# Kernel optimization log

Measured on AMD Instinct MI355X. Metric: run time of the kernel, lower is better.

Reference implementation:

```python
import math
import jax, jax.numpy as jnp
import numpy as np

N = 2048          # batch size
D = 256           # embedding_dim
MEM = 16384       # memory_size
ANOMALY_WEIGHT = 1.0
TEMP = 0.1
MOMENTUM = 0.01
NCLS = 2          # binary phishing labels -> max(labels.max()+1, 2) == 2


def setup_inputs() -> dict:
    key = jax.random.key(0)
    ks = jax.random.split(key, 10)
    s = 1.0 / math.sqrt(D)  # nn.Linear default init range
    return {
        'z': jax.random.normal(ks[0], (N, D), jnp.float32),
        'labels': jax.random.randint(ks[1], (N,), 0, NCLS),
        'memory': jax.random.normal(ks[2], (MEM, D), jnp.float32),
        'memory_weights': jax.random.uniform(ks[3], (MEM,), jnp.float32),
        'running_mean': jnp.zeros((D,), jnp.float32),
        'running_cov': jnp.eye(D, dtype=jnp.float32),
        'Wq': jax.random.uniform(ks[4], (D, D), jnp.float32, -s, s),
        'bq': jax.random.uniform(ks[5], (D,), jnp.float32, -s, s),
        'Wk': jax.random.uniform(ks[6], (D, D), jnp.float32, -s, s),
        'bk': jax.random.uniform(ks[7], (D,), jnp.float32, -s, s),
        'Wv': jax.random.uniform(ks[8], (D, D), jnp.float32, -s, s),
        'bv': jax.random.uniform(ks[9], (D,), jnp.float32, -s, s),
    }


def reference(z, labels, memory, memory_weights, running_mean, running_cov,
              Wq, bq, Wk, bk, Wv, bv):
    # ---- update(z.detach(), labels): entire update path is detached in torch ----
    z_sg = jax.lax.stop_gradient(z)

    # _update_stats: EMA of batch mean / covariance (done before importance)
    mu = z_sg.mean(axis=0)                                  # [D]
    zc = z_sg - mu
    cov = zc.T @ zc / max(N - 1, 1)                         # [D, D]
    rm = (1.0 - MOMENTUM) * running_mean + MOMENTUM * mu
    rc = (1.0 - MOMENTUM) * running_cov + MOMENTUM * cov

    # _mahalanobis with updated running stats
    c = z_sg - rm
    cov_inv = jnp.linalg.inv(rc + 1e-6 * jnp.eye(D, dtype=rc.dtype))
    dist = jnp.sqrt(jnp.clip(jnp.einsum('nd,de,ne->n', c, cov_inv, c), 1e-8))
    a_norm = (dist - dist.min()) / (dist.max() - dist.min() + 1e-8)

    # _mi_proxy: KL(batch label dist || uniform), broadcast to all items
    counts = jnp.zeros((NCLS,), z.dtype).at[labels].add(1.0)
    p = counts / jnp.clip(counts.sum(), 1.0)
    # p / uniform == p * NCLS; clip inside log for safety (both classes present)
    kl = jnp.clip((p * jnp.log(jnp.clip(p * NCLS, 1e-8))).sum(), 0.0)
    importance = (1.0 + ANOMALY_WEIGHT * a_norm) * kl       # [N]

    # serial top-1 priority-queue eviction, in descending-importance order
    order = jnp.argsort(-importance)
    z_ord = z_sg[order]
    imp_ord = importance[order]

    def evict_step(state, inp):
        mem, w = state
        zi, imp = inp
        j = jnp.argmin(w)                   # weakest memory slot
        rep = imp > w[j]
        mem = mem.at[j].set(jnp.where(rep, zi, mem[j]))
        w = w.at[j].set(jnp.where(rep, imp, w[j]))
        return (mem, w), None

    (mem, _), _ = jax.lax.scan(evict_step, (memory, memory_weights), (z_ord, imp_ord))

    # ---- query(z): cross-attention over the (full) updated memory ----
    Q = z @ Wq.T + bq                       # [N, D]
    K = mem @ Wk.T + bk                     # [MEM, D]
    V = mem @ Wv.T + bv                     # [MEM, D]
    sc = (Q @ K.T) / math.sqrt(D)           # [N, MEM]
    attn = jax.nn.softmax(sc / TEMP, axis=-1)
    return z + 0.5 * (attn @ V)
```

## Files before the change

kernel.cpp:

```cpp
#include <hip/hip_runtime.h>
#include <math.h>

#define NB   2048
#define DE   256
#define MEMN 16384
#define CAND_CAP 256
#define FSPL 32
#define FKPS 512
#define FIT  16

typedef __attribute__((ext_vector_type(8)))  short  short8;
typedef __attribute__((ext_vector_type(16))) float  float16;
typedef __attribute__((ext_vector_type(4)))  unsigned uint4v;
typedef __attribute__((ext_vector_type(2)))  unsigned uint2v;

static const size_t OFF_QB   = 0;
static const size_t OFF_KB   = 262144;
static const size_t OFF_VTB  = 2359296;
static const size_t OFF_LP   = 4456448;
static const size_t OFF_OPB  = 4521984;
static const size_t SO_APART = 0;
static const size_t SO_A     = 1048576;
static const size_t SO_MUP   = 1114112;
static const size_t SO_DIST  = 1130496;

__device__ inline unsigned short f2bf(float f) {
  unsigned u = __float_as_uint(f);
  unsigned r = (u + 0x7fffu + ((u >> 16) & 1u)) >> 16;
  return (unsigned short)r;
}
__device__ inline float bf2f(unsigned short s) {
  return __uint_as_float((unsigned)s << 16);
}

__device__ inline unsigned cvtpk_bf16(float lo, float hi) {
  unsigned r;
  asm("v_cvt_pk_bf16_f32 %0, %1, %2" : "=v"(r) : "v"(lo), "v"(hi));
  return r;
}
__device__ inline short8 pack8_bf16(float4 f0, float4 f1) {
  uint4v u = {cvtpk_bf16(f0.x, f0.y), cvtpk_bf16(f0.z, f0.w),
              cvtpk_bf16(f1.x, f1.y), cvtpk_bf16(f1.z, f1.w)};
  return __builtin_bit_cast(short8, u);
}

__device__ inline void halfswap(unsigned& lo, unsigned& hi, int h) {
#if __has_builtin(__builtin_amdgcn_permlane32_swap)
  (void)h;
  uint2v r = __builtin_amdgcn_permlane32_swap(lo, hi, false, false);
  lo = r.x; hi = r.y;
#else
  unsigned a = (unsigned)__shfl_xor((int)lo, 32, 64);
  unsigned b = (unsigned)__shfl_xor((int)hi, 32, 64);
  unsigned nlo = (h == 0) ? lo : b;
  unsigned nhi = (h == 0) ? a  : hi;
  lo = nlo; hi = nhi;
#endif
}

__device__ inline void bitonic_sort_u64(unsigned long long* key, int n, int tid, int nth) {
  for (int k = 2; k <= n; k <<= 1) {
    for (int j = k >> 1; j > 0; j >>= 1) {
      __syncthreads();
      for (int i = tid; i < n; i += nth) {
        int ixj = i ^ j;
        if (ixj > i) {
          unsigned long long a = key[i], b = key[ixj];
          bool up = ((i & k) == 0);
          if ((a > b) == up) { key[i] = b; key[ixj] = a; }
        }
      }
    }
  }
  __syncthreads();
}

__global__ __launch_bounds__(256) void covmu_kernel(const float* __restrict__ z,
                                                    float* __restrict__ Apart,
                                                    float* __restrict__ mup,
                                                    const float* __restrict__ Wq,
                                                    const float* __restrict__ bq,
                                                    unsigned short* __restrict__ Qbf) {
  int f = blockIdx.x;
  int tid = threadIdx.x;
  if (f >= 320) {
    __shared__ unsigned short Bsh[64 * 264];
    int g = f - 320;
    int gx = g & 15, gy = g >> 4;
    int w = tid >> 6, lane = tid & 63;
    int m = lane & 31, h = lane >> 5;
    int arow = gx * 128 + w * 32 + m;
    int n0 = gy * 64;
    short8 af[16];
#pragma unroll
    for (int kc = 0; kc < 16; ++kc) {
      const float* src = &z[(size_t)arow * DE + kc * 16 + h * 8];
      af[kc] = pack8_bf16(*(const float4*)&src[0], *(const float4*)&src[4]);
    }
    {
      int r = tid >> 2, q = tid & 3;
      const float* src = &Wq[(size_t)(n0 + r) * DE + q * 64];
      unsigned short* dst = &Bsh[r * 264 + q * 64];
#pragma unroll
      for (int j = 0; j < 8; ++j)
        *(short8*)&dst[j * 8] = pack8_bf16(*(const float4*)&src[j * 8],
                                           *(const float4*)&src[j * 8 + 4]);
    }
    __syncthreads();
    float16 a0 = {}, a1 = {};
#pragma unroll
    for (int kc = 0; kc < 16; ++kc) {
      short8 b0 = *(const short8*)&Bsh[(0 * 32 + m) * 264 + kc * 16 + h * 8];
      short8 b1 = *(const short8*)&Bsh[(1 * 32 + m) * 264 + kc * 16 + h * 8];
      a0 = __builtin_amdgcn_mfma_f32_32x32x16_bf16(af[kc], b0, a0, 0, 0, 0);
      a1 = __builtin_amdgcn_mfma_f32_32x32x16_bf16(af[kc], b1, a1, 0, 0, 0);
    }
#pragma unroll
    for (int r = 0; r < 16; ++r) {
      int rr = (r & 3) + 8 * (r >> 2) + 4 * h;
      int orow = gx * 128 + w * 32 + rr;
      int oc0 = n0 + m, oc1 = n0 + 32 + m;
      Qbf[(size_t)orow * DE + oc0] = f2bf(a0[r] + bq[oc0]);
      Qbf[(size_t)orow * DE + oc1] = f2bf(a1[r] + bq[oc1]);
    }
    return;
  }
  if (f >= 256) {
    int b = f - 256;
    int r0 = b * 32;
    float s = 0.f;
    for (int r = 0; r < 32; ++r) s += z[(size_t)(r0 + r) * DE + tid];
    mup[b * DE + tid] = s;
    return;
  }
  __shared__ float As[16][68];
  __shared__ float Bs[16][68];
  int tx = tid & 15, ty = tid >> 4;
  int i0 = (f & 3) * 64, j0 = ((f >> 2) & 3) * 64;
  int slice = f >> 4;
  int nbase = slice * 128;
  float acc[4][4] = {};
  for (int nt = 0; nt < 8; ++nt) {
    int n0 = nbase + nt * 16;
    for (int e = tid; e < 1024; e += 256) {
      int c = e & 63, nn = e >> 6;
      As[nn][c] = z[(size_t)(n0 + nn) * DE + i0 + c];
      Bs[nn][c] = z[(size_t)(n0 + nn) * DE + j0 + c];
    }
    __syncthreads();
#pragma unroll
    for (int nn = 0; nn < 16; ++nn) {
      float4 a4 = *(const float4*)&As[nn][ty * 4];
      float4 b4 = *(const float4*)&Bs[nn][tx * 4];
      acc[0][0] += a4.x*b4.x; acc[0][1] += a4.x*b4.y; acc[0][2] += a4.x*b4.z; acc[0][3] += a4.x*b4.w;
      acc[1][0] += a4.y*b4.x; acc[1][1] += a4.y*b4.y; acc[1][2] += a4.y*b4.z; acc[1][3] += a4.y*b4.w;
      acc[2][0] += a4.z*b4.x; acc[2][1] += a4.z*b4.y; acc[2][2] += a4.z*b4.z; acc[2][3] += a4.z*b4.w;
      acc[3][0] += a4.w*b4.x; acc[3][1] += a4.w*b4.y; acc[3][2] += a4.w*b4.z; acc[3][3] += a4.w*b4.w;
    }
    __syncthreads();
  }
  float* dstA = &Apart[(size_t)slice * 65536];
  for (int r = 0; r < 4; ++r) {
    int i = i0 + ty * 4 + r;
    for (int c = 0; c < 4; ++c) {
      int j = j0 + tx * 4 + c;
      dstA[(size_t)i * DE + j] = acc[r][c];
    }
  }
}

__global__ __launch_bounds__(256) void covred_kernel(const float* __restrict__ Apart,
                                                     float* __restrict__ A) {
  int e0 = (blockIdx.x * 256 + threadIdx.x) * 4;
  float4 s = {0.f, 0.f, 0.f, 0.f};
#pragma unroll
  for (int sl = 0; sl < 16; ++sl) {
    float4 v = *(const float4*)&Apart[(size_t)sl * 65536 + e0];
    s.x += v.x; s.y += v.y; s.z += v.z; s.w += v.w;
  }
  *(float4*)&A[e0] = s;
}

__global__ __launch_bounds__(256) void dist_kernel(const float* __restrict__ z,
                                                   const float* __restrict__ rmean,
                                                   const float* __restrict__ mup,
                                                   const float* __restrict__ ZtZ,
                                                   const float* __restrict__ rcov,
                                                   float* __restrict__ dist) {
  __shared__ float cc[8][256];
  __shared__ float mus[256];
  __shared__ float4 red[256];
  int n0 = blockIdx.x * 8, i = threadIdx.x;
  float s = 0.f;
  for (int b = 0; b < 64; ++b) s += mup[b * DE + i];
  mus[i] = s;
  float rmi = 0.99f * rmean[i] + 0.01f * s * (1.0f / (float)NB);
#pragma unroll
  for (int r = 0; r < 8; ++r) cc[r][i] = z[(size_t)(n0 + r) * DE + i] - rmi;
  __syncthreads();
  const float c1 = 0.01f / (float)(NB - 1);
  const float invN = 1.0f / (float)NB;
  float musi = mus[i];
  float u[8] = {};
#pragma unroll 4
  for (int j = 0; j < DE; ++j) {
    float base = 0.99f * rcov[(size_t)j * DE + i] +
                 c1 * (ZtZ[(size_t)j * DE + i] - mus[j] * musi * invN);
    float e = -base;
    if (j == i) e += 1.0f - 1e-6f;
#pragma unroll
    for (int r = 0; r < 8; ++r) u[r] += e * cc[r][j];
  }
  {
    float4 v;
    v.x = cc[0][i] * (cc[0][i] + u[0]) + u[0] * u[0];
    v.y = cc[1][i] * (cc[1][i] + u[1]) + u[1] * u[1];
    v.z = cc[2][i] * (cc[2][i] + u[2]) + u[2] * u[2];
    v.w = cc[3][i] * (cc[3][i] + u[3]) + u[3] * u[3];
    red[i] = v;
    __syncthreads();
    for (int sH = 128; sH > 0; sH >>= 1) {
      if (i < sH) {
        float4 a = red[i], b = red[i + sH];
        a.x += b.x; a.y += b.y; a.z += b.z; a.w += b.w;
        red[i] = a;
      }
      __syncthreads();
    }
    if (i < 4) {
      float4 tt = red[0];
      float d = (i == 0) ? tt.x : (i == 1) ? tt.y : (i == 2) ? tt.z : tt.w;
      dist[n0 + i] = sqrtf(fmaxf(d, 1e-8f));
    }
    __syncthreads();
  }
  {
    float4 v;
    v.x = cc[4][i] * (cc[4][i] + u[4]) + u[4] * u[4];
    v.y = cc[5][i] * (cc[5][i] + u[5]) + u[5] * u[5];
    v.z = cc[6][i] * (cc[6][i] + u[6]) + u[6] * u[6];
    v.w = cc[7][i] * (cc[7][i] + u[7]) + u[7] * u[7];
    red[i] = v;
    __syncthreads();
    for (int sH = 128; sH > 0; sH >>= 1) {
      if (i < sH) {
        float4 a = red[i], b = red[i + sH];
        a.x += b.x; a.y += b.y; a.z += b.z; a.w += b.w;
        red[i] = a;
      }
      __syncthreads();
    }
    if (i < 4) {
      float4 tt = red[0];
      float d = (i == 0) ? tt.x : (i == 1) ? tt.y : (i == 2) ? tt.z : tt.w;
      dist[n0 + 4 + i] = sqrtf(fmaxf(d, 1e-8f));
    }
  }
}

__global__ __launch_bounds__(1024) void update_kernel(const float* __restrict__ dist,
                                                      const int* __restrict__ labels,
                                                      const float* __restrict__ weights,
                                                      const float* __restrict__ z,
                                                      float* __restrict__ memory) {
  __shared__ unsigned long long ikeys[NB];
  __shared__ unsigned long long ck[CAND_CAP];
  __shared__ unsigned long long gmin[16];
  __shared__ int slots[CAND_CAP], srcs[CAND_CAP];
  __shared__ float smin[16], smax[16];
  __shared__ int scnt[16];
  __shared__ float s_kl, s_dmin, s_inv;
  __shared__ int s_ccnt, s_m, s_stop, s_bg;
  int t = threadIdx.x;
  int wid = t >> 6, lane = t & 63;

  float mn = 1e30f, mx = -1e30f; int c1 = 0;
  for (int n = t; n < NB; n += 1024) {
    float d = dist[n];
    mn = fminf(mn, d); mx = fmaxf(mx, d);
    c1 += labels[n];
  }
#pragma unroll
  for (int o = 32; o > 0; o >>= 1) {
    mn = fminf(mn, __shfl_xor(mn, o, 64));
    mx = fmaxf(mx, __shfl_xor(mx, o, 64));
    c1 += __shfl_xor(c1, o, 64);
  }
  if (lane == 0) { smin[wid] = mn; smax[wid] = mx; scnt[wid] = c1; }
  if (t == 0) { s_ccnt = 0; s_m = 0; s_stop = 0; }
  __syncthreads();
  if (t == 0) {
    float a = 1e30f, b = -1e30f; int cc = 0;
    for (int i = 0; i < 16; ++i) { a = fminf(a, smin[i]); b = fmaxf(b, smax[i]); cc += scnt[i]; }
    float p1 = (float)cc / (float)NB;
    float p0 = (float)(NB - cc) / (float)NB;
    float kl = p0 * logf(fmaxf(2.f * p0, 1e-8f)) + p1 * logf(fmaxf(2.f * p1, 1e-8f));
    s_kl = fmaxf(kl, 0.f);
    s_dmin = a;
    s_inv = 1.0f / (b - a + 1e-8f);
  }
  __syncthreads();
  float kl = s_kl;

  for (int n = t; n < NB; n += 1024) {
    float imp = (1.0f + (dist[n] - s_dmin) * s_inv) * kl;
    ikeys[n] = ((unsigned long long)(unsigned)(~__float_as_uint(imp)) << 32) | (unsigned)n;
  }
  float thresh = 2.f * kl;
  for (int j = t; j < MEMN; j += 1024) {
    float wv = weights[j];
    if (wv < thresh) {
      int p = atomicAdd(&s_ccnt, 1);
      if (p < CAND_CAP) ck[p] = ((unsigned long long)__float_as_uint(wv) << 32) | (unsigned)j;
    }
  }
  __syncthreads();
  int C = s_ccnt; if (C > CAND_CAP) C = CAND_CAP;
  for (int i = t; i < CAND_CAP; i += 1024)
    if (i >= C) ck[i] = 0xFFFFFFFFFFFFFFFFULL;
  __syncthreads();
  if (C <= 64) {
    if (wid == 0) {
      unsigned long long key = (lane < C) ? ck[lane] : 0xFFFFFFFFFFFFFFFFULL;
      int rank = 0;
      for (int j = 0; j < 64; ++j) {
        unsigned long long o = (unsigned long long)__shfl((long long)key, j, 64);
        rank += (o < key) || (o == key && j < lane);
      }
      if (lane < C) ck[rank] = key;
    }
    __syncthreads();
  } else {
    bitonic_sort_u64(ck, CAND_CAP, t, 1024);
  }

  {
    unsigned long long a = ikeys[wid * 128 + lane];
    unsigned long long b = ikeys[wid * 128 + 64 + lane];
    unsigned long long mm = a < b ? a : b;
#pragma unroll
    for (int o = 32; o > 0; o >>= 1) {
      unsigned long long ot = (unsigned long long)__shfl_xor((long long)mm, o, 64);
      if (ot < mm) mm = ot;
    }
    if (lane == 0) gmin[wid] = mm;
  }
  __syncthreads();

  float prevv = 0.f;
  for (int i = 0; i < C; ++i) {
    if (t == 0) {
      unsigned long long best = 0xFFFFFFFFFFFFFFFFULL;
      for (int g = 0; g < 16; ++g) if (gmin[g] < best) best = gmin[g];
      float im = __uint_as_float(~(unsigned)(best >> 32));
      float wv = __uint_as_float((unsigned)(ck[i] >> 32));
      bool ok = (im > wv) && (i == 0 || prevv >= wv);
      if (ok) {
        int idx = (int)(best & 0xffffffffULL);
        slots[s_m] = (int)(ck[i] & 0xffffffffULL);
        srcs[s_m]  = idx;
        s_m++;
        prevv = im;
        ikeys[idx] = 0xFFFFFFFFFFFFFFFFULL;
        s_bg = idx >> 7;
      } else {
        s_stop = 1; s_bg = -1;
      }
    }
    __syncthreads();
    if (s_stop) break;
    if (wid == s_bg) {
      unsigned long long a = ikeys[wid * 128 + lane];
      unsigned long long b = ikeys[wid * 128 + 64 + lane];
      unsigned long long mm = a < b ? a : b;
#pragma unroll
      for (int o = 32; o > 0; o >>= 1) {
        unsigned long long ot = (unsigned long long)__shfl_xor((long long)mm, o, 64);
        if (ot < mm) mm = ot;
      }
      if (lane == 0) gmin[wid] = mm;
    }
    __syncthreads();
  }
  int m = s_m;
  for (int e = t; e < m * DE; e += 1024) {
    int i = e >> 8, d = e & 255;
    memory[(size_t)slots[i] * DE + d] = z[(size_t)srcs[i] * DE + d];
  }
}

__global__ __launch_bounds__(256, 1) void qkv_kernel(
    const float* __restrict__ memory,
    const float* __restrict__ Wk, const float* __restrict__ bk,
    const float* __restrict__ Wv, const float* __restrict__ bv,
    unsigned short* __restrict__ Kbf, unsigned short* __restrict__ Vtb) {
  __shared__ unsigned short Bsh[64 * 264];
  int flat = blockIdx.x;
  int tid = threadIdx.x;
  int w = tid >> 6, lane = tid & 63;
  int m = lane & 31, h = lane >> 5;

  if (flat < 128) {
    int gx = flat;
    int arow = gx * 128 + w * 32 + m;
    short8 af[16];
#pragma unroll
    for (int kc = 0; kc < 16; ++kc) {
      const float* src = &memory[(size_t)arow * DE + kc * 16 + h * 8];
      af[kc] = pack8_bf16(*(const float4*)&src[0], *(const float4*)&src[4]);
    }
    for (int g4 = 0; g4 < 4; ++g4) {
      int n0 = g4 * 64;
      __syncthreads();
      {
        int r = tid >> 2, q = tid & 3;
        const float* src = &Wk[(size_t)(n0 + r) * DE + q * 64];
        unsigned short* dst = &Bsh[r * 264 + q * 64];
#pragma unroll
        for (int j = 0; j < 8; ++j)
          *(short8*)&dst[j * 8] = pack8_bf16(*(const float4*)&src[j * 8],
                                             *(const float4*)&src[j * 8 + 4]);
      }
      __syncthreads();
      float16 a0 = {}, a1 = {};
#pragma unroll
      for (int kc = 0; kc < 16; ++kc) {
        short8 b0 = *(const short8*)&Bsh[(0 * 32 + m) * 264 + kc * 16 + h * 8];
        short8 b1 = *(const short8*)&Bsh[(1 * 32 + m) * 264 + kc * 16 + h * 8];
        a0 = __builtin_amdgcn_mfma_f32_32x32x16_bf16(af[kc], b0, a0, 0, 0, 0);
        a1 = __builtin_amdgcn_mfma_f32_32x32x16_bf16(af[kc], b1, a1, 0, 0, 0);
      }
#pragma unroll
      for (int r = 0; r < 16; ++r) {
        int rr = (r & 3) + 8 * (r >> 2) + 4 * h;
        int orow = gx * 128 + w * 32 + rr;
        int oc0 = n0 + m, oc1 = n0 + 32 + m;
        Kbf[(size_t)orow * DE + oc0] = f2bf(a0[r] + bk[oc0]);
        Kbf[(size_t)orow * DE + oc1] = f2bf(a1[r] + bk[oc1]);
      }
    }
  } else {
    int gy = flat - 128;
    int n0 = gy * 64;
    {
      int r = tid >> 2, q = tid & 3;
      const float* src = &memory[(size_t)(n0 + r) * DE + q * 64];
      unsigned short* dst = &Bsh[r * 264 + q * 64];
#pragma unroll
      for (int j = 0; j < 8; ++j)
        *(short8*)&dst[j * 8] = pack8_bf16(*(const float4*)&src[j * 8],
                                           *(const float4*)&src[j * 8 + 4]);
    }
    __syncthreads();
    for (int gxv = 0; gxv < 2; ++gxv) {
      short8 af[16];
#pragma unroll
      for (int kc = 0; kc < 16; ++kc) {
        const float* src = &Wv[(size_t)(gxv * 128 + w * 32 + m) * DE + kc * 16 + h * 8];
        af[kc] = pack8_bf16(*(const float4*)&src[0], *(const float4*)&src[4]);
      }
      float16 a0 = {}, a1 = {};
#pragma unroll
      for (int kc = 0; kc < 16; ++kc) {
        short8 b0 = *(const short8*)&Bsh[(0 * 32 + m) * 264 + kc * 16 + h * 8];
        short8 b1 = *(const short8*)&Bsh[(1 * 32 + m) * 264 + kc * 16 + h * 8];
        a0 = __builtin_amdgcn_mfma_f32_32x32x16_bf16(af[kc], b0, a0, 0, 0, 0);
        a1 = __builtin_amdgcn_mfma_f32_32x32x16_bf16(af[kc], b1, a1, 0, 0, 0);
      }
#pragma unroll
      for (int r = 0; r < 16; ++r) {
        int rr = (r & 3) + 8 * (r >> 2) + 4 * h;
        int orow = gxv * 128 + w * 32 + rr;
        int oc0 = n0 + m, oc1 = n0 + 32 + m;
        Vtb[(size_t)(oc0 >> 5) * 8192 + (size_t)orow * 32 + (oc0 & 31)] = f2bf(a0[r] + bv[orow]);
        Vtb[(size_t)(oc1 >> 5) * 8192 + (size_t)orow * 32 + (oc1 & 31)] = f2bf(a1[r] + bv[orow]);
      }
    }
  }
}

__global__ __launch_bounds__(512, 2) void flash_kernel(
    const unsigned short* __restrict__ Qb, const unsigned short* __restrict__ Kb,
    const unsigned short* __restrict__ Vtb, unsigned short* __restrict__ Opb,
    float* __restrict__ Lp) {
  __shared__ unsigned short Ks[32 * 264];
  __shared__ unsigned short Vs[256 * 40];

  int tid = threadIdx.x;
  int w = tid >> 6, lane = tid & 63;
  int m = lane & 31, h = lane >> 5;
  int sp = blockIdx.x, qg = blockIdx.y;
  int myrow = qg * 256 + w * 32 + m;

  short8 qf[16];
#pragma unroll
  for (int kc = 0; kc < 16; ++kc)
    qf[kc] = *(const short8*)&Qb[(size_t)myrow * DE + kc * 16 + h * 8];

  float16 O[8] = {};
  float lacc = 0.f;

  short8 kreg[2], vreg[2];
#define LOAD_TILES(kb_)                                                              \
  {                                                                                  \
    int kb = (kb_);                                                                  \
    _Pragma("unroll")                                                                \
    for (int i = 0; i < 2; ++i) {                                                    \
      int c = i * 512 + tid, kr = c >> 5, kcol = c & 31;                             \
      kreg[i] = *(const short8*)&Kb[(size_t)(kb + kr) * DE + kcol * 8];              \
    }                                                                                \
    const unsigned short* vg = &Vtb[(size_t)((kb) >> 5) * 8192];                     \
    _Pragma("unroll")                                                                \
    for (int i = 0; i < 2; ++i) {                                                    \
      int c = i * 512 + tid;                                                         \
      vreg[i] = *(const short8*)&vg[c * 8];                                          \
    }                                                                                \
  }
#define STORE_TILES()                                                                \
  {                                                                                  \
    _Pragma("unroll")                                                                \
    for (int i = 0; i < 2; ++i) {                                                    \
      int c = i * 512 + tid, kr = c >> 5, kcol = c & 31;                             \
      *(short8*)&Ks[kr * 264 + kcol * 8] = kreg[i];                                  \
    }                                                                                \
    _Pragma("unroll")                                                                \
    for (int i = 0; i < 2; ++i) {                                                    \
      int c = i * 512 + tid, dr = c >> 2, dc = c & 3;                                \
      *(short8*)&Vs[dr * 40 + dc * 8] = vreg[i];                                     \
    }                                                                                \
  }

  LOAD_TILES(sp * FKPS);

  for (int it = 0; it < FIT; ++it) {
    __syncthreads();
    STORE_TILES();
    if (it + 1 < FIT) LOAD_TILES(sp * FKPS + (it + 1) * 32);
    __syncthreads();

    float16 s = {};
    __builtin_amdgcn_s_setprio(1);
#pragma unroll
    for (int kc = 0; kc < 16; ++kc) {
      short8 b0 = *(const short8*)&Ks[m * 264 + kc * 16 + h * 8];
      s = __builtin_amdgcn_mfma_f32_32x32x16_bf16(b0, qf[kc], s, 0, 0, 0);
    }
    __builtin_amdgcn_s_setprio(0);

    float p[16];
#pragma unroll
    for (int r = 0; r < 16; ++r)
      p[r] = exp2f(fmaf(s[r], 0.90168440f, -16.0f));

    lacc += ((p[0] + p[1]) + (p[2] + p[3])) + ((p[4] + p[5]) + (p[6] + p[7])) +
            ((p[8] + p[9]) + (p[10] + p[11])) + ((p[12] + p[13]) + (p[14] + p[15]));

    unsigned c0 = cvtpk_bf16(p[0],  p[1]);
    unsigned c1 = cvtpk_bf16(p[2],  p[3]);
    unsigned c2 = cvtpk_bf16(p[4],  p[5]);
    unsigned c3 = cvtpk_bf16(p[6],  p[7]);
    unsigned c4 = cvtpk_bf16(p[8],  p[9]);
    unsigned c5 = cvtpk_bf16(p[10], p[11]);
    unsigned c6 = cvtpk_bf16(p[12], p[13]);
    unsigned c7 = cvtpk_bf16(p[14], p[15]);
    halfswap(c0, c2, h);
    halfswap(c1, c3, h);
    halfswap(c4, c6, h);
    halfswap(c5, c7, h);
    uint4v w0v = {c0, c1, c2, c3};
    uint4v w1v = {c4, c5, c6, c7};
    short8 pa0 = __builtin_bit_cast(short8, w0v);
    short8 pa1 = __builtin_bit_cast(short8, w1v);

    __builtin_amdgcn_s_setprio(1);
#pragma unroll
    for (int ct = 0; ct < 8; ++ct) {
      short8 vb0 = *(const short8*)&Vs[(ct * 32 + m) * 40 + h * 8];
      short8 vb1 = *(const short8*)&Vs[(ct * 32 + m) * 40 + 16 + h * 8];
      O[ct] = __builtin_amdgcn_mfma_f32_32x32x16_bf16(pa0, vb0, O[ct], 0, 0, 0);
      O[ct] = __builtin_amdgcn_mfma_f32_32x32x16_bf16(pa1, vb1, O[ct], 0, 0, 0);
    }
    __builtin_amdgcn_s_setprio(0);
  }
#undef LOAD_TILES
#undef STORE_TILES

  size_t ob = ((size_t)sp * NB + qg * 256 + w * 32) * DE;
#pragma unroll
  for (int ct = 0; ct < 8; ++ct)
#pragma unroll
    for (int r = 0; r < 16; ++r) {
      int rr = (r & 3) + 8 * (r >> 2) + 4 * h;
      Opb[ob + (size_t)rr * DE + ct * 32 + m] = f2bf(O[ct][r]);
    }
  float ltot = lacc + __shfl_xor(lacc, 32, 64);
  if (h == 0)
    Lp[sp * NB + qg * 256 + w * 32 + m] = ltot;
}

__global__ __launch_bounds__(256) void combine_kernel(const float* __restrict__ z,
                                                      const unsigned short* __restrict__ Opb,
                                                      const float* __restrict__ Lp,
                                                      float* __restrict__ out) {
  int t = threadIdx.x;
  int n = blockIdx.x * 8 + (t >> 5);
  int c0 = (t & 31) * 8;
  float num[8] = {};
  float den = 0.f;
#pragma unroll
  for (int s = 0; s < FSPL; ++s) {
    den += Lp[s * NB + n];
    short8 v = *(const short8*)&Opb[((size_t)s * NB + n) * DE + c0];
#pragma unroll
    for (int j = 0; j < 8; ++j) num[j] += bf2f((unsigned short)v[j]);
  }
  size_t base = (size_t)n * DE + c0;
  float4 o0, o1;
  o0.x = z[base + 0] + 0.5f * num[0] / den;
  o0.y = z[base + 1] + 0.5f * num[1] / den;
  o0.z = z[base + 2] + 0.5f * num[2] / den;
  o0.w = z[base + 3] + 0.5f * num[3] / den;
  o1.x = z[base + 4] + 0.5f * num[4] / den;
  o1.y = z[base + 5] + 0.5f * num[5] / den;
  o1.z = z[base + 6] + 0.5f * num[6] / den;
  o1.w = z[base + 7] + 0.5f * num[7] / den;
  *(float4*)&out[base] = o0;
  *(float4*)&out[base + 4] = o1;
}

extern "C" void kernel_launch(void* const* d_in, const int* in_sizes, int n_in,
                              void* d_out, int out_size, void* d_ws, size_t ws_size,
                              hipStream_t stream) {
  (void)in_sizes; (void)n_in; (void)out_size; (void)ws_size;
  const float* z       = (const float*)d_in[0];
  const int*   labels  = (const int*)d_in[1];
  float*       memory  = (float*)d_in[2];
  const float* weights = (const float*)d_in[3];
  const float* rmean   = (const float*)d_in[4];
  const float* rcov    = (const float*)d_in[5];
  const float* Wq      = (const float*)d_in[6];
  const float* bq      = (const float*)d_in[7];
  const float* Wk      = (const float*)d_in[8];
  const float* bk      = (const float*)d_in[9];
  const float* Wv      = (const float*)d_in[10];
  const float* bv      = (const float*)d_in[11];
  float* out = (float*)d_out;
  float* ws  = (float*)d_ws;

  unsigned short* Qbf = (unsigned short*)(ws + OFF_QB);
  unsigned short* Kbf = (unsigned short*)(ws + OFF_KB);
  unsigned short* Vtb = (unsigned short*)(ws + OFF_VTB);
  float* Lp           = ws + OFF_LP;
  unsigned short* Opb = (unsigned short*)(ws + OFF_OPB);
  float* SB    = ws + OFF_OPB;
  float* Apart = SB + SO_APART;
  float* A     = SB + SO_A;
  float* mup   = SB + SO_MUP;
  float* dist  = SB + SO_DIST;

  covmu_kernel<<<384, 256, 0, stream>>>(z, Apart, mup, Wq, bq, Qbf);
  covred_kernel<<<64, 256, 0, stream>>>(Apart, A);
  dist_kernel<<<NB / 8, 256, 0, stream>>>(z, rmean, mup, A, rcov, dist);
  update_kernel<<<1, 1024, 0, stream>>>(dist, labels, weights, z, memory);
  qkv_kernel<<<384, 256, 0, stream>>>(memory, Wk, bk, Wv, bv, Kbf, Vtb);
  flash_kernel<<<dim3(FSPL, NB / 256), 512, 0, stream>>>(Qbf, Kbf, Vtb, Opb, Lp);
  combine_kernel<<<NB / 8, 256, 0, stream>>>(z, Opb, Lp, out);
}
```

Baseline: 215.5 us.

## Project K/V from pre-update memory up front, then patch only evicted slots

K and V are now computed from the original memory inside the merged front kernel, alongside the covariance, mean and Q work, so they no longer wait for the serial update kernel. The update kernel records which memory slots it replaced, and a small fixup kernel recomputes the K/V rows for just those slots in fp32 before bf16 rounding. This takes the full memory projection off the critical path after the single-block update and overlaps it with the front-end work. The cost is a larger front launch and an extra small kernel with uncoalesced weight reads; patched rows are rounded slightly differently from the MFMA-computed rows.

```diff
diff --git a/kernel.cpp b/kernel.cpp
--- a/kernel.cpp
+++ b/kernel.cpp
@@ -23,6 +23,7 @@
 static const size_t SO_A     = 1048576;
 static const size_t SO_MUP   = 1114112;
 static const size_t SO_DIST  = 1130496;
+static const size_t SO_SLOTS = 1132544;
 
 __device__ inline unsigned short f2bf(float f) {
   unsigned u = __float_as_uint(f);
@@ -75,20 +76,67 @@
   __syncthreads();
 }
 
-__global__ __launch_bounds__(256) void covmu_kernel(const float* __restrict__ z,
-                                                    float* __restrict__ Apart,
-                                                    float* __restrict__ mup,
-                                                    const float* __restrict__ Wq,
-                                                    const float* __restrict__ bq,
-                                                    unsigned short* __restrict__ Qbf) {
+__global__ __launch_bounds__(256) void front_kernel(
+    const float* __restrict__ z, float* __restrict__ Apart, float* __restrict__ mup,
+    const float* __restrict__ Wq, const float* __restrict__ bq,
+    unsigned short* __restrict__ Qbf,
+    const float* __restrict__ memory,
+    const float* __restrict__ Wk, const float* __restrict__ bk,
+    const float* __restrict__ Wv, const float* __restrict__ bv,
+    unsigned short* __restrict__ Kbf, unsigned short* __restrict__ Vtb) {
+  __shared__ __align__(16) unsigned char lds_raw[33792];
   int f = blockIdx.x;
   int tid = threadIdx.x;
-  if (f >= 320) {
-    __shared__ unsigned short Bsh[64 * 264];
+  int w = tid >> 6, lane = tid & 63;
+  int m = lane & 31, h = lane >> 5;
+
+  if (f < 256) {
+    float (*As)[68] = (float(*)[68])lds_raw;
+    float (*Bs)[68] = (float(*)[68])(lds_raw + 4352);
+    int tx = tid & 15, ty = tid >> 4;
+    int i0 = (f & 3) * 64, j0 = ((f >> 2) & 3) * 64;
+    int slice = f >> 4;
+    int nbase = slice * 128;
+    float acc[4][4] = {};
+    for (int nt = 0; nt < 8; ++nt) {
+      int n0 = nbase + nt * 16;
+      for (int e = tid; e < 1024; e += 256) {
+        int c = e & 63, nn = e >> 6;
+        As[nn][c] = z[(size_t)(n0 + nn) * DE + i0 + c];
+        Bs[nn][c] = z[(size_t)(n0 + nn) * DE + j0 + c];
+      }
+      __syncthreads();
+#pragma unroll
+      for (int nn = 0; nn < 16; ++nn) {
+        float4 a4 = *(const float4*)&As[nn][ty * 4];
+        float4 b4 = *(const float4*)&Bs[nn][tx * 4];
+        acc[0][0] += a4.x*b4.x; acc[0][1] += a4.x*b4.y; acc[0][2] += a4.x*b4.z; acc[0][3] += a4.x*b4.w;
+        acc[1][0] += a4.y*b4.x; acc[1][1] += a4.y*b4.y; acc[1][2] += a4.y*b4.z; acc[1][3] += a4.y*b4.w;
+        acc[2][0] += a4.z*b4.x; acc[2][1] += a4.z*b4.y; acc[2][2] += a4.z*b4.z; acc[2][3] += a4.z*b4.w;
+        acc[3][0] += a4.w*b4.x; acc[3][1] += a4.w*b4.y; acc[3][2] += a4.w*b4.z; acc[3][3] += a4.w*b4.w;
+      }
+      __syncthreads();
+    }
+    float* dstA = &Apart[(size_t)slice * 65536];
+    for (int r = 0; r < 4; ++r) {
+      int i = i0 + ty * 4 + r;
+      for (int c = 0; c < 4; ++c)
+        dstA[(size_t)i * DE + j0 + tx * 4 + c] = acc[r][c];
+    }
+    return;
+  }
+  if (f < 320) {
+    int b = f - 256;
+    int r0 = b * 32;
+    float s = 0.f;
+    for (int r = 0; r < 32; ++r) s += z[(size_t)(r0 + r) * DE + tid];
+    mup[b * DE + tid] = s;
+    return;
+  }
+  unsigned short* Bsh = (unsigned short*)lds_raw;
+  if (f < 384) {
     int g = f - 320;
     int gx = g & 15, gy = g >> 4;
-    int w = tid >> 6, lane = tid & 63;
-    int m = lane & 31, h = lane >> 5;
     int arow = gx * 128 + w * 32 + m;
     int n0 = gy * 64;
     short8 af[16];
@@ -125,46 +173,83 @@
     }
     return;
   }
-  if (f >= 256) {
-    int b = f - 256;
-    int r0 = b * 32;
-    float s = 0.f;
-    for (int r = 0; r < 32; ++r) s += z[(size_t)(r0 + r) * DE + tid];
-    mup[b * DE + tid] = s;
+  if (f < 512) {
+    int gx = f - 384;
+    int arow = gx * 128 + w * 32 + m;
+    short8 af[16];
+#pragma unroll
+    for (int kc = 0; kc < 16; ++kc) {
+      const float* src = &memory[(size_t)arow * DE + kc * 16 + h * 8];
+      af[kc] = pack8_bf16(*(const float4*)&src[0], *(const float4*)&src[4]);
+    }
+    for (int g4 = 0; g4 < 4; ++g4) {
+      int n0 = g4 * 64;
+      __syncthreads();
+      {
+        int r = tid >> 2, q = tid & 3;
+        const float* src = &Wk[(size_t)(n0 + r) * DE + q * 64];
+        unsigned short* dst = &Bsh[r * 264 + q * 64];
+#pragma unroll
+        for (int j = 0; j < 8; ++j)
+          *(short8*)&dst[j * 8] = pack8_bf16(*(const float4*)&src[j * 8],
+                                             *(const float4*)&src[j * 8 + 4]);
+      }
+      __syncthreads();
+      float16 a0 = {}, a1 = {};
+#pragma unroll
+      for (int kc = 0; kc < 16; ++kc) {
+        short8 b0 = *(const short8*)&Bsh[(0 * 32 + m) * 264 + kc * 16 + h * 8];
+        short8 b1 = *(const short8*)&Bsh[(1 * 32 + m) * 264 + kc * 16 + h * 8];
+        a0 = __builtin_amdgcn_mfma_f32_32x32x16_bf16(af[kc], b0, a0, 0, 0, 0);
+        a1 = __builtin_amdgcn_mfma_f32_32x32x16_bf16(af[kc], b1, a1, 0, 0, 0);
+      }
+#pragma unroll
+      for (int r = 0; r < 16; ++r) {
+        int rr = (r & 3) + 8 * (r >> 2) + 4 * h;
+        int orow = gx * 128 + w * 32 + rr;
+        int oc0 = n0 + m, oc1 = n0 + 32 + m;
+        Kbf[(size_t)orow * DE + oc0] = f2bf(a0[r] + bk[oc0]);
+        Kbf[(size_t)orow * DE + oc1] = f2bf(a1[r] + bk[oc1]);
+      }
+    }
     return;
   }
-  __shared__ float As[16][68];
-  __shared__ float Bs[16][68];
-  int tx = tid & 15, ty = tid >> 4;
-  int i0 = (f & 3) * 64, j0 = ((f >> 2) & 3) * 64;
-  int slice = f >> 4;
-  int nbase = slice * 128;
-  float acc[4][4] = {};
-  for (int nt = 0; nt < 8; ++nt) {
-    int n0 = nbase + nt * 16;
-    for (int e = tid; e < 1024; e += 256) {
-      int c = e & 63, nn = e >> 6;
-      As[nn][c] = z[(size_t)(n0 + nn) * DE + i0 + c];
-      Bs[nn][c] = z[(size_t)(n0 + nn) * DE + j0 + c];
-    }
-    __syncthreads();
-#pragma unroll
-    for (int nn = 0; nn < 16; ++nn) {
-      float4 a4 = *(const float4*)&As[nn][ty * 4];
-      float4 b4 = *(const float4*)&Bs[nn][tx * 4];
-      acc[0][0] += a4.x*b4.x; acc[0][1] += a4.x*b4.y; acc[0][2] += a4.x*b4.z; acc[0][3] += a4.x*b4.w;
-      acc[1][0] += a4.y*b4.x; acc[1][1] += a4.y*b4.y; acc[1][2] += a4.y*b4.z; acc[1][3] += a4.y*b4.w;
-      acc[2][0] += a4.z*b4.x; acc[2][1] += a4.z*b4.y; acc[2][2] += a4.z*b4.z; acc[2][3] += a4.z*b4.w;
-      acc[3][0] += a4.w*b4.x; acc[3][1] += a4.w*b4.y; acc[3][2] += a4.w*b4.z; acc[3][3] += a4.w*b4.w;
-    }
-    __syncthreads();
-  }
-  float* dstA = &Apart[(size_t)slice * 65536];
-  for (int r = 0; r < 4; ++r) {
-    int i = i0 + ty * 4 + r;
-    for (int c = 0; c < 4; ++c) {
-      int j = j0 + tx * 4 + c;
-      dstA[(size_t)i * DE + j] = acc[r][c];
+  {
+    int gy = f - 512;
+    int n0 = gy * 64;
+    {
+      int r = tid >> 2, q = tid & 3;
+      const float* src = &memory[(size_t)(n0 + r) * DE + q * 64];
+      unsigned short* dst = &Bsh[r * 264 + q * 64];
+#pragma unroll
+      for (int j = 0; j < 8; ++j)
+        *(short8*)&dst[j * 8] = pack8_bf16(*(const float4*)&src[j * 8],
+                                           *(const float4*)&src[j * 8 + 4]);
+    }
+    __syncthreads();
+    for (int gxv = 0; gxv < 2; ++gxv) {
+      short8 af[16];
+#pragma unroll
+      for (int kc = 0; kc < 16; ++kc) {
+        const float* src = &Wv[(size_t)(gxv * 128 + w * 32 + m) * DE + kc * 16 + h * 8];
+        af[kc] = pack8_bf16(*(const float4*)&src[0], *(const float4*)&src[4]);
+      }
+      float16 a0 = {}, a1 = {};
+#pragma unroll
+      for (int kc = 0; kc < 16; ++kc) {
+        short8 b0 = *(const short8*)&Bsh[(0 * 32 + m) * 264 + kc * 16 + h * 8];
+        short8 b1 = *(const short8*)&Bsh[(1 * 32 + m) * 264 + kc * 16 + h * 8];
+        a0 = __builtin_amdgcn_mfma_f32_32x32x16_bf16(af[kc], b0, a0, 0, 0, 0);
+        a1 = __builtin_amdgcn_mfma_f32_32x32x16_bf16(af[kc], b1, a1, 0, 0, 0);
+      }
+#pragma unroll
+      for (int r = 0; r < 16; ++r) {
+        int rr = (r & 3) + 8 * (r >> 2) + 4 * h;
+        int orow = gxv * 128 + w * 32 + rr;
+        int oc0 = n0 + m, oc1 = n0 + 32 + m;
+        Vtb[(size_t)(oc0 >> 5) * 8192 + (size_t)orow * 32 + (oc0 & 31)] = f2bf(a0[r] + bv[orow]);
+        Vtb[(size_t)(oc1 >> 5) * 8192 + (size_t)orow * 32 + (oc1 & 31)] = f2bf(a1[r] + bv[orow]);
+      }
     }
   }
 }
@@ -262,7 +347,8 @@
                                                       const int* __restrict__ labels,
                                                       const float* __restrict__ weights,
                                                       const float* __restrict__ z,
-                                                      float* __restrict__ memory) {
+                                                      float* __restrict__ memory,
+                                                      int* __restrict__ slotsOut) {
   __shared__ unsigned long long ikeys[NB];
   __shared__ unsigned long long ck[CAND_CAP];
   __shared__ unsigned long long gmin[16];
@@ -383,100 +469,38 @@
     __syncthreads();
   }
   int m = s_m;
+  if (t == 0) slotsOut[0] = m;
+  if (t < m) slotsOut[1 + t] = slots[t];
   for (int e = t; e < m * DE; e += 1024) {
     int i = e >> 8, d = e & 255;
     memory[(size_t)slots[i] * DE + d] = z[(size_t)srcs[i] * DE + d];
   }
 }
 
-__global__ __launch_bounds__(256, 1) void qkv_kernel(
-    const float* __restrict__ memory,
-    const float* __restrict__ Wk, const float* __restrict__ bk,
-    const float* __restrict__ Wv, const float* __restrict__ bv,
-    unsigned short* __restrict__ Kbf, unsigned short* __restrict__ Vtb) {
-  __shared__ unsigned short Bsh[64 * 264];
-  int flat = blockIdx.x;
-  int tid = threadIdx.x;
-  int w = tid >> 6, lane = tid & 63;
-  int m = lane & 31, h = lane >> 5;
-
-  if (flat < 128) {
-    int gx = flat;
-    int arow = gx * 128 + w * 32 + m;
-    short8 af[16];
-#pragma unroll
-    for (int kc = 0; kc < 16; ++kc) {
-      const float* src = &memory[(size_t)arow * DE + kc * 16 + h * 8];
-      af[kc] = pack8_bf16(*(const float4*)&src[0], *(const float4*)&src[4]);
-    }
-    for (int g4 = 0; g4 < 4; ++g4) {
-      int n0 = g4 * 64;
-      __syncthreads();
-      {
-        int r = tid >> 2, q = tid & 3;
-        const float* src = &Wk[(size_t)(n0 + r) * DE + q * 64];
-        unsigned short* dst = &Bsh[r * 264 + q * 64];
-#pragma unroll
-        for (int j = 0; j < 8; ++j)
-          *(short8*)&dst[j * 8] = pack8_bf16(*(const float4*)&src[j * 8],
-                                             *(const float4*)&src[j * 8 + 4]);
-      }
-      __syncthreads();
-      float16 a0 = {}, a1 = {};
-#pragma unroll
-      for (int kc = 0; kc < 16; ++kc) {
-        short8 b0 = *(const short8*)&Bsh[(0 * 32 + m) * 264 + kc * 16 + h * 8];
-        short8 b1 = *(const short8*)&Bsh[(1 * 32 + m) * 264 + kc * 16 + h * 8];
-        a0 = __builtin_amdgcn_mfma_f32_32x32x16_bf16(af[kc], b0, a0, 0, 0, 0);
-        a1 = __builtin_amdgcn_mfma_f32_32x32x16_bf16(af[kc], b1, a1, 0, 0, 0);
-      }
-#pragma unroll
-      for (int r = 0; r < 16; ++r) {
-        int rr = (r & 3) + 8 * (r >> 2) + 4 * h;
-        int orow = gx * 128 + w * 32 + rr;
-        int oc0 = n0 + m, oc1 = n0 + 32 + m;
-        Kbf[(size_t)orow * DE + oc0] = f2bf(a0[r] + bk[oc0]);
-        Kbf[(size_t)orow * DE + oc1] = f2bf(a1[r] + bk[oc1]);
-      }
-    }
-  } else {
-    int gy = flat - 128;
-    int n0 = gy * 64;
-    {
-      int r = tid >> 2, q = tid & 3;
-      const float* src = &memory[(size_t)(n0 + r) * DE + q * 64];
-      unsigned short* dst = &Bsh[r * 264 + q * 64];
-#pragma unroll
-      for (int j = 0; j < 8; ++j)
-        *(short8*)&dst[j * 8] = pack8_bf16(*(const float4*)&src[j * 8],
-                                           *(const float4*)&src[j * 8 + 4]);
-    }
-    __syncthreads();
-    for (int gxv = 0; gxv < 2; ++gxv) {
-      short8 af[16];
-#pragma unroll
-      for (int kc = 0; kc < 16; ++kc) {
-        const float* src = &Wv[(size_t)(gxv * 128 + w * 32 + m) * DE + kc * 16 + h * 8];
-        af[kc] = pack8_bf16(*(const float4*)&src[0], *(const float4*)&src[4]);
-      }
-      float16 a0 = {}, a1 = {};
-#pragma unroll
-      for (int kc = 0; kc < 16; ++kc) {
-        short8 b0 = *(const short8*)&Bsh[(0 * 32 + m) * 264 + kc * 16 + h * 8];
-        short8 b1 = *(const short8*)&Bsh[(1 * 32 + m) * 264 + kc * 16 + h * 8];
-        a0 = __builtin_amdgcn_mfma_f32_32x32x16_bf16(af[kc], b0, a0, 0, 0, 0);
-        a1 = __builtin_amdgcn_mfma_f32_32x32x16_bf16(af[kc], b1, a1, 0, 0, 0);
-      }
-#pragma unroll
-      for (int r = 0; r < 16; ++r) {
-        int rr = (r & 3) + 8 * (r >> 2) + 4 * h;
-        int orow = gxv * 128 + w * 32 + rr;
-        int oc0 = n0 + m, oc1 = n0 + 32 + m;
-        Vtb[(size_t)(oc0 >> 5) * 8192 + (size_t)orow * 32 + (oc0 & 31)] = f2bf(a0[r] + bv[orow]);
-        Vtb[(size_t)(oc1 >> 5) * 8192 + (size_t)orow * 32 + (oc1 & 31)] = f2bf(a1[r] + bv[orow]);
-      }
-    }
-  }
+__global__ __launch_bounds__(256) void fixup_kernel(const int* __restrict__ slotsOut,
+                                                    const float* __restrict__ memory,
+                                                    const float* __restrict__ Wk,
+                                                    const float* __restrict__ bk,
+                                                    const float* __restrict__ Wv,
+                                                    const float* __restrict__ bv,
+                                                    unsigned short* __restrict__ Kbf,
+                                                    unsigned short* __restrict__ Vtb) {
+  int cnt = slotsOut[0];
+  if ((int)blockIdx.x >= cnt) return;
+  int slot = slotsOut[1 + blockIdx.x];
+  __shared__ float mrow[256];
+  int j = threadIdx.x;
+  mrow[j] = memory[(size_t)slot * DE + j];
+  __syncthreads();
+  float kj = 0.f, vj = 0.f;
+#pragma unroll 4
+  for (int d = 0; d < DE; ++d) {
+    float md = mrow[d];
+    kj = fmaf(md, Wk[(size_t)j * DE + d], kj);
+    vj = fmaf(md, Wv[(size_t)j * DE + d], vj);
+  }
+  Kbf[(size_t)slot * DE + j] = f2bf(kj + bk[j]);
+  Vtb[(size_t)(slot >> 5) * 8192 + (size_t)j * 32 + (slot & 31)] = f2bf(vj + bv[j]);
 }
 
 __global__ __launch_bounds__(512, 2) void flash_kernel(
@@ -657,12 +681,14 @@
   float* A     = SB + SO_A;
   float* mup   = SB + SO_MUP;
   float* dist  = SB + SO_DIST;
-
-  covmu_kernel<<<384, 256, 0, stream>>>(z, Apart, mup, Wq, bq, Qbf);
+  int*   slotsOut = (int*)(SB + SO_SLOTS);
+
+  front_kernel<<<768, 256, 0, stream>>>(z, Apart, mup, Wq, bq, Qbf,
+                                        memory, Wk, bk, Wv, bv, Kbf, Vtb);
   covred_kernel<<<64, 256, 0, stream>>>(Apart, A);
   dist_kernel<<<NB / 8, 256, 0, stream>>>(z, rmean, mup, A, rcov, dist);
-  update_kernel<<<1, 1024, 0, stream>>>(dist, labels, weights, z, memory);
-  qkv_kernel<<<384, 256, 0, stream>>>(memory, Wk, bk, Wv, bv, Kbf, Vtb);
+  update_kernel<<<1, 1024, 0, stream>>>(dist, labels, weights, z, memory, slotsOut);
+  fixup_kernel<<<CAND_CAP, 256, 0, stream>>>(slotsOut, memory, Wk, bk, Wv, bv, Kbf, Vtb);
   flash_kernel<<<dim3(FSPL, NB / 256), 512, 0, stream>>>(Qbf, Kbf, Vtb, Opb, Lp);
   combine_kernel<<<NB / 8, 256, 0, stream>>>(z, Opb, Lp, out);
 }
```

Measured after the change: 226.7 us. 1.05x slower.
